# Performance work log

Hardware: AMD Instinct MI355X
Metric: run time of the kernel (lower is better)

The kernel has to match this reference:

```python
import jax, jax.numpy as jnp
import numpy as np

B, S, V, D, E, L = 4, 256, 50000, 300, 128, 20  # batch, seq, vocab, embed, encoder_size, labels


def _gru(x, h0, wih, whh, bih, bhh):
    """Unidirectional torch-style GRU. x: [B,S,Din], h0: [B,H]. Returns ([B,S,H], [B,H])."""
    gx = jnp.einsum('bsd,hd->bsh', x, wih) + bih  # precompute all input projections [B,S,3H]

    def step(h, gx_t):
        gh = h @ whh.T + bhh
        xr, xz, xn = jnp.split(gx_t, 3, axis=-1)
        hr, hz, hn = jnp.split(gh, 3, axis=-1)
        r = jax.nn.sigmoid(xr + hr)
        z = jax.nn.sigmoid(xz + hz)
        n = jnp.tanh(xn + r * hn)
        h2 = (1.0 - z) * n + z * h
        return h2, h2

    hT, hs = jax.lax.scan(step, h0, jnp.swapaxes(gx, 0, 1))
    return jnp.swapaxes(hs, 0, 1), hT


def _bigru(x, h0, pf, pb):
    """Bidirectional GRU. h0: [2,B,H]. Returns ([B,S,2H], [2,B,H])."""
    of, hf = _gru(x, h0[0], *pf)
    ob, hb = _gru(x[:, ::-1], h0[1], *pb)
    return jnp.concatenate([of, ob[:, ::-1]], axis=-1), jnp.stack([hf, hb])


def reference(inputs, emb,
              enc_wih_f, enc_whh_f, enc_bih_f, enc_bhh_f,
              enc_wih_b, enc_whh_b, enc_bih_b, enc_bhh_b,
              hid_wih_f, hid_whh_f, hid_bih_f, hid_bhh_f,
              hid_wih_b, hid_whh_b, hid_bih_b, hid_bhh_b,
              agg_wih_f, agg_whh_f, agg_bih_f, agg_bhh_f,
              agg_wih_b, agg_whh_b, agg_bih_b, agg_bhh_b,
              Wc1, Wc2, vc, Wb, Wd, vd, Wm, vm, Ws, vs, Wp, vp, Wpred):
    x = emb[inputs]                                # [B,S,D]
    b = x.shape[0]
    h0 = jnp.zeros((2, b, E), x.dtype)
    hp, hidden = _bigru(x, h0,
                        (enc_wih_f, enc_whh_f, enc_bih_f, enc_bhh_f),
                        (enc_wih_b, enc_whh_b, enc_bih_b, enc_bhh_b))   # [B,S,2E]
    hq, _ = _bigru(hp, hidden,
                   (hid_wih_f, hid_whh_f, hid_bih_f, hid_bhh_f),
                   (hid_wih_b, hid_whh_b, hid_bih_b, hid_bhh_b))        # [B,S,2E]

    # ptc: additive attention, score = vc . tanh(Wc1 hp_k + Wc2 hq_q)
    s1 = jnp.einsum('bkd,ed->bke', hp, Wc1)
    s2 = jnp.einsum('bqd,ed->bqe', hq, Wc2)
    sc = jnp.einsum('bqke,e->bqk', jnp.tanh(s1[:, None] + s2[:, :, None]), vc)
    ptc = jnp.einsum('bqk,bkd->bqd', jax.nn.softmax(sc, -1), hp)

    # ptb: bilinear attention, score = hq_q . (Wb hp_k)
    sc = jnp.einsum('bqd,bkd->bqk', hq, jnp.einsum('bkd,ed->bke', hp, Wb))
    ptb = jnp.einsum('bqk,bkd->bqd', jax.nn.softmax(sc, -1), hp)

    # ptd: score = vd . tanh(Wd (hp_k * hq_q))
    sc = jnp.einsum('bqke,e->bqk', jnp.tanh(jnp.einsum('bqkd,ed->bqke', hp[:, None] * hq[:, :, None], Wd)), vd)
    ptd = jnp.einsum('bqk,bkd->bqd', jax.nn.softmax(sc, -1), hp)

    # ptm: score = vm . tanh(Wm (hp_k - hq_q))
    sc = jnp.einsum('bqke,e->bqk', jnp.tanh(jnp.einsum('bqkd,ed->bqke', hp[:, None] - hq[:, :, None], Wm)), vm)
    ptm = jnp.einsum('bqk,bkd->bqd', jax.nn.softmax(sc, -1), hp)

    # pts: self, score = vs . tanh(Ws (hq_k * hq_q))
    sc = jnp.einsum('bqke,e->bqk', jnp.tanh(jnp.einsum('bqkd,ed->bqke', hq[:, None] * hq[:, :, None], Ws)), vs)
    pts = jnp.einsum('bqk,bkd->bqd', jax.nn.softmax(sc, -1), hq)

    agg = jnp.concatenate([hq, pts, ptc, ptd, ptb, ptm], axis=-1)  # [B,S,12E]
    agg_rep, _ = _bigru(agg, jnp.zeros((2, b, E), x.dtype),
                        (agg_wih_f, agg_whh_f, agg_bih_f, agg_bhh_f),
                        (agg_wih_b, agg_whh_b, agg_bih_b, agg_bhh_b))  # [B,S,2E]

    # pooled query rl over hq
    sj = jnp.einsum('bse,e->bs', jnp.tanh(jnp.einsum('bsd,ed->bse', hq, Wp)), vp)
    rl = jnp.einsum('bs,bsd->bd', jax.nn.softmax(sj, -1), hq)       # [B,2E]

    # final pooling over agg_rep (note: no tanh here, matching source)
    sc = jnp.einsum('bse,e->bs',
                    jnp.einsum('bsd,ed->bse', agg_rep, Wc1) + jnp.einsum('bd,ed->be', rl, Wc2)[:, None],
                    vc)
    rr = jnp.einsum('bs,bsd->bd', jax.nn.softmax(sc, -1), agg_rep)  # [B,2E]
    return jax.nn.sigmoid(rr @ Wpred.T)                              # [B,labels]


def setup_inputs() -> dict:
    key = jax.random.key(0)
    ks = iter(jax.random.split(key, 64))
    f = lambda *s: jax.random.normal(next(ks), s, jnp.float32) * 0.05
    H3 = 3 * E
    return dict(
        inputs=jax.random.randint(next(ks), (B, S), 0, V),
        emb=f(V, D),
        enc_wih_f=f(H3, D), enc_whh_f=f(H3, E), enc_bih_f=f(H3), enc_bhh_f=f(H3),
        enc_wih_b=f(H3, D), enc_whh_b=f(H3, E), enc_bih_b=f(H3), enc_bhh_b=f(H3),
        hid_wih_f=f(H3, 2 * E), hid_whh_f=f(H3, E), hid_bih_f=f(H3), hid_bhh_f=f(H3),
        hid_wih_b=f(H3, 2 * E), hid_whh_b=f(H3, E), hid_bih_b=f(H3), hid_bhh_b=f(H3),
        agg_wih_f=f(H3, 12 * E), agg_whh_f=f(H3, E), agg_bih_f=f(H3), agg_bhh_f=f(H3),
        agg_wih_b=f(H3, 12 * E), agg_whh_b=f(H3, E), agg_bih_b=f(H3), agg_bhh_b=f(H3),
        Wc1=f(E, 2 * E), Wc2=f(E, 2 * E), vc=f(E),
        Wb=f(2 * E, 2 * E),
        Wd=f(E, 2 * E), vd=f(E),
        Wm=f(E, 2 * E), vm=f(E),
        Ws=f(E, 2 * E), vs=f(E),
        Wp=f(E, 2 * E), vp=f(E),
        Wpred=f(L, 2 * E),
    )
```

## Files before the change

### kernel.cpp

```cpp
#include <hip/hip_runtime.h>
#include <math.h>

#define BB 4
#define SS 256
#define DD 300
#define DP 304
#define EE 128
#define LL 20
#define H3 384
#define D2 256
#define D12 1536

typedef __attribute__((ext_vector_type(8)))  short short8;
typedef __attribute__((ext_vector_type(16))) float f32x16;

__device__ __forceinline__ float tanh_fast(float x){
  float e = __expf(2.f*x);
  return 1.f - 2.f/(e+1.f);
}
__device__ __forceinline__ float sigmoidf_(float x){ return 1.f/(1.f+__expf(-x)); }
__device__ __forceinline__ float bf16_to_f(unsigned u){ return __builtin_bit_cast(float, u<<16); }
__device__ __forceinline__ float bf16hi_to_f(unsigned u){ return __builtin_bit_cast(float, u & 0xFFFF0000u); }
__device__ __forceinline__ unsigned bf16_rne(float f){
  unsigned u = __builtin_bit_cast(unsigned, f);
  return (u + 0x7FFFu + ((u>>16)&1u)) >> 16;
}
__device__ __forceinline__ unsigned pack_bf16x2(float lo, float hi){
  return bf16_rne(lo) | (bf16_rne(hi)<<16);
}

__global__ void k_cvt_bf16(const float* __restrict__ src, unsigned short* __restrict__ dst, int n2){
  int i = blockIdx.x*blockDim.x + threadIdx.x;
  if (i < n2){
    float2 f = *(const float2*)(src + 2*i);
    *(unsigned*)(dst + 2*i) = pack_bf16x2(f.x, f.y);
  }
}

struct CvtSeg { const float* src; unsigned short* dst; int rows, Ks, Kd; };
struct CvtArgs { CvtSeg s[13]; };
__global__ void k_cvt_weights(CvtArgs a){
  CvtSeg sg = a.s[blockIdx.y];
  int p = blockIdx.x*256 + threadIdx.x;
  int Kd2 = sg.Kd>>1;
  int npairs = sg.rows*Kd2;
  if (p >= npairs) return;
  int row = p/Kd2, kk = (p - row*Kd2)*2;
  float f0 = (kk   < sg.Ks)? sg.src[(size_t)row*sg.Ks+kk  ] : 0.f;
  float f1 = (kk+1 < sg.Ks)? sg.src[(size_t)row*sg.Ks+kk+1] : 0.f;
  *(unsigned*)(sg.dst + (size_t)row*sg.Kd + kk) = pack_bf16x2(f0,f1);
}

__global__ void k_embed(const int* __restrict__ inp, const float* __restrict__ emb,
                        unsigned short* __restrict__ xb){
  int row = blockIdx.x;
  int idx = inp[row];
  const float* src = emb + (size_t)idx*DD;
  unsigned short* dst = xb + (size_t)row*DP;
  int p = threadIdx.x;
  if (p < DP/2){
    float f0 = (2*p   < DD)? src[2*p  ] : 0.f;
    float f1 = (2*p+1 < DD)? src[2*p+1] : 0.f;
    *(unsigned*)(dst + 2*p) = pack_bf16x2(f0,f1);
  }
}

__global__ void k_init2(float* __restrict__ gf, const float* __restrict__ bf,
                        float* __restrict__ gb, const float* __restrict__ bb){
  int row = blockIdx.x, n = threadIdx.x;
  gf[(size_t)row*H3+n] = bf[n];
  gb[(size_t)row*H3+n] = bb[n];
}

__global__ __launch_bounds__(64) void k_mmbf(
    const unsigned short* __restrict__ X, const unsigned short* __restrict__ W,
    const float* __restrict__ bias, float* __restrict__ out,
    int N, int K, int kspan){
  int lane=threadIdx.x, col=lane&31, half=lane>>5;
  int n0=blockIdx.x*32, m0=blockIdx.y*64;
  int ks=blockIdx.z*kspan, ke=ks+kspan; if (ke>K) ke=K;
  const unsigned short* pa0 = X + (size_t)(m0+col)*K + half*8;
  const unsigned short* pa1 = pa0 + (size_t)32*K;
  const unsigned short* pb  = W + (size_t)(n0+col)*K + half*8;
  f32x16 acc0={}, acc1={};
  #pragma unroll 2
  for (int k=ks;k<ke;k+=16){
    short8 a0=__builtin_bit_cast(short8, *(const uint4*)(pa0+k));
    short8 a1=__builtin_bit_cast(short8, *(const uint4*)(pa1+k));
    short8 bv=__builtin_bit_cast(short8, *(const uint4*)(pb +k));
    acc0=__builtin_amdgcn_mfma_f32_32x32x16_bf16(a0,bv,acc0,0,0,0);
    acc1=__builtin_amdgcn_mfma_f32_32x32x16_bf16(a1,bv,acc1,0,0,0);
  }
  int cn = n0+col;
  if (gridDim.z==1){
    float bn = bias? bias[cn] : 0.f;
    #pragma unroll
    for (int r=0;r<16;r++){
      int row=(r&3)+8*(r>>2)+4*half;
      out[(size_t)(m0+row)*N+cn]    = acc0[r]+bn;
      out[(size_t)(m0+32+row)*N+cn] = acc1[r]+bn;
    }
  } else {
    #pragma unroll
    for (int r=0;r<16;r++){
      int row=(r&3)+8*(r>>2)+4*half;
      atomicAdd(&out[(size_t)(m0+row)*N+cn],    acc0[r]);
      atomicAdd(&out[(size_t)(m0+32+row)*N+cn], acc1[r]);
    }
  }
}

__global__ __launch_bounds__(512, 1) void k_gru_scan(const float* __restrict__ gxf, const float* __restrict__ gxb,
                          const float* __restrict__ whhf, const float* __restrict__ whhb,
                          const float* __restrict__ bhhf, const float* __restrict__ bhhb,
                          const float* __restrict__ h0,
                          float* __restrict__ out,
                          float* __restrict__ hT){
  int b=blockIdx.x, dir=blockIdx.y, tid=threadIdx.x;
  const float* gx  = dir? gxb : gxf;
  const float* whh = dir? whhb : whhf;
  const float* bhh = dir? bhhb : bhhf;
  int r = tid>>2, part = tid&3, phase = r&7;
  float4 w_r[8], w_z[8], w_n[8];
  #pragma unroll
  for (int j=0;j<8;j++){
    int jj=(j+phase)&7;
    int off = part*32 + jj*4;
    w_r[j] = *(const float4*)&whh[(size_t)r*EE        + off];
    w_z[j] = *(const float4*)&whh[(size_t)(r+128)*EE  + off];
    w_n[j] = *(const float4*)&whh[(size_t)(r+256)*EE  + off];
  }
  float b_r=bhh[r], b_z=bhh[r+128], b_n=bhh[r+256];
  __shared__ __align__(16) float h[2][EE];
  float hprev = h0? h0[((size_t)dir*BB+b)*EE + r] : 0.f;
  if (part==0) h[0][r] = hprev;
  float xr=0.f,xz=0.f,xn=0.f;
  {
    int s0 = dir? (SS-1) : 0;
    const float* g0 = gx + ((size_t)b*SS+s0)*H3;
    if (part==0){ xr=g0[r]; xz=g0[EE+r]; xn=g0[2*EE+r]; }
  }
  __syncthreads();
  int cur=0;
  for (int t=0;t<SS;t++){
    int s = dir? (SS-1-t) : t;
    float ar=0.f, az=0.f, an=0.f;
    #pragma unroll
    for (int j=0;j<8;j++){
      int jj=(j+phase)&7;
      float4 hv = *(const float4*)&h[cur][part*32 + jj*4];
      ar += w_r[j].x*hv.x + w_r[j].y*hv.y + w_r[j].z*hv.z + w_r[j].w*hv.w;
      az += w_z[j].x*hv.x + w_z[j].y*hv.y + w_z[j].z*hv.z + w_z[j].w*hv.w;
      an += w_n[j].x*hv.x + w_n[j].y*hv.y + w_n[j].z*hv.z + w_n[j].w*hv.w;
    }
    ar += __shfl_xor(ar,1); ar += __shfl_xor(ar,2);
    az += __shfl_xor(az,1); az += __shfl_xor(az,2);
    an += __shfl_xor(an,1); an += __shfl_xor(an,2);
    if (part==0){
      float rg = sigmoidf_(xr + ar + b_r);
      float zg = sigmoidf_(xz + az + b_z);
      float ng = tanh_fast(xn + rg*(an + b_n));
      float h2 = (1.f-zg)*ng + zg*hprev;
      hprev = h2;
      h[cur^1][r] = h2;
      out[((size_t)b*SS+s)*D2 + dir*EE + r] = h2;
      if (t+1<SS){
        int sn = dir? (SS-2-t) : (t+1);
        const float* gn = gx + ((size_t)b*SS+sn)*H3;
        xr=gn[r]; xz=gn[EE+r]; xn=gn[2*EE+r];
      }
    }
    cur^=1;
    __syncthreads();
  }
  if (hT && part==0) hT[((size_t)dir*BB+b)*EE+r]=hprev;
}

__global__ void k_copy_hq(const unsigned short* __restrict__ hqb, unsigned short* __restrict__ aggb){
  int row=blockIdx.x;
  aggb[(size_t)row*D12 + threadIdx.x] = hqb[(size_t)row*D2 + threadIdx.x];
}

__device__ __forceinline__ void softmax256(float val, float* red, float* p){
  int tid=threadIdx.x;
  red[tid]=val; __syncthreads();
  for (int st=128; st>0; st>>=1){ if (tid<st) red[tid]=fmaxf(red[tid],red[tid+st]); __syncthreads(); }
  float mx=red[0]; __syncthreads();
  float ex=__expf(val-mx); red[tid]=ex; __syncthreads();
  for (int st=128; st>0; st>>=1){ if (tid<st) red[tid]+=red[tid+st]; __syncthreads(); }
  float inv=1.f/red[0];
  p[tid]=ex*inv; __syncthreads();
}

__global__ __launch_bounds__(256) void k_attn_add(const float* __restrict__ A, const float* __restrict__ Bq,
                          const float* __restrict__ v, float sign,
                          const float* __restrict__ V, unsigned short* __restrict__ aggout, int off){
  __shared__ __align__(16) float bq[EE];
  __shared__ __align__(16) float vv[EE];
  __shared__ float p[SS]; __shared__ float red[SS];
  int q=blockIdx.x, b=blockIdx.y, tid=threadIdx.x;
  if (tid<EE){ bq[tid]=sign*Bq[((size_t)b*SS+q)*EE+tid]; vv[tid]=v[tid]; }
  __syncthreads();
  const float* Ar = A + ((size_t)b*SS+tid)*EE;
  float s=0.f;
  #pragma unroll
  for (int e=0;e<EE;e+=4){
    float4 a=*(const float4*)(Ar+e);
    float4 bb=*(const float4*)(bq+e);
    float4 vw=*(const float4*)(vv+e);
    s += vw.x*tanh_fast(a.x+bb.x)+vw.y*tanh_fast(a.y+bb.y)+vw.z*tanh_fast(a.z+bb.z)+vw.w*tanh_fast(a.w+bb.w);
  }
  softmax256(s, red, p);
  const float* V0 = V + (size_t)b*SS*D2;
  float o=0.f;
  for (int k=0;k<SS;k++) o += p[k]*V0[(size_t)k*D2+tid];
  aggout[((size_t)b*SS+q)*D12 + off + tid] = (unsigned short)bf16_rne(o);
}

__global__ __launch_bounds__(256) void k_attn_bil(const float* __restrict__ Pb, const float* __restrict__ hq,
                          const float* __restrict__ V, unsigned short* __restrict__ aggout, int off){
  __shared__ __align__(16) float hqq[D2];
  __shared__ float p[SS]; __shared__ float red[SS];
  int q=blockIdx.x, b=blockIdx.y, tid=threadIdx.x;
  hqq[tid]=hq[((size_t)b*SS+q)*D2+tid];
  __syncthreads();
  const float* Pr = Pb + ((size_t)b*SS+tid)*D2;
  float s=0.f;
  #pragma unroll
  for (int d=0;d<D2;d+=4){
    float4 a=*(const float4*)(Pr+d);
    float4 hh=*(const float4*)(hqq+d);
    s += a.x*hh.x+a.y*hh.y+a.z*hh.z+a.w*hh.w;
  }
  softmax256(s, red, p);
  const float* V0 = V + (size_t)b*SS*D2;
  float o=0.f;
  for (int k=0;k<SS;k++) o += p[k]*V0[(size_t)k*D2+tid];
  aggout[((size_t)b*SS+q)*D12 + off + tid] = (unsigned short)bf16_rne(o);
}

__global__ __launch_bounds__(256, 2) void k_mulattn_fused(
    const unsigned short* __restrict__ keysb,
    const float* __restrict__ qm,
    const unsigned short* __restrict__ Wb,
    const float* __restrict__ v,
    const float* __restrict__ V,
    unsigned short* __restrict__ aggout, int off){
  __shared__ __align__(16) float qrow[D2];
  __shared__ __align__(16) float vrow[EE];
  __shared__ float scq[SS];
  __shared__ float red[SS];
  __shared__ float p[SS];
  int q=blockIdx.x, b=blockIdx.y, tid=threadIdx.x;
  int wave=tid>>6, lane=tid&63;
  size_t bS = (size_t)b*SS;
  qrow[tid]=qm[(bS+q)*D2+tid];
  if (tid<EE) vrow[tid]=v[tid];
  __syncthreads();

  f32x16 acc[2][4]={};
  int m0 = wave*64;
  int col = lane&31, half = lane>>5;
  const unsigned short* krow0 = keysb + (bS + m0 + col)*D2 + half*8;
  const unsigned short* krow1 = krow0 + 32*D2;
  const unsigned short* wrow[4];
  #pragma unroll
  for (int n=0;n<4;n++) wrow[n] = Wb + (size_t)(n*32+col)*D2 + half*8;

  for (int d0=0; d0<D2; d0+=16){
    float4 qsA = *(const float4*)&qrow[d0 + half*8];
    float4 qsB = *(const float4*)&qrow[d0 + half*8 + 4];
    short8 bfrag[4];
    #pragma unroll
    for (int n=0;n<4;n++) bfrag[n] = __builtin_bit_cast(short8, *(const uint4*)(wrow[n]+d0));
    #pragma unroll
    for (int i=0;i<2;i++){
      uint4 raw = *(const uint4*)((i? krow1:krow0) + d0);
      float f0=bf16_to_f(raw.x)*qsA.x, f1=bf16hi_to_f(raw.x)*qsA.y;
      float f2=bf16_to_f(raw.y)*qsA.z, f3=bf16hi_to_f(raw.y)*qsA.w;
      float f4=bf16_to_f(raw.z)*qsB.x, f5=bf16hi_to_f(raw.z)*qsB.y;
      float f6=bf16_to_f(raw.w)*qsB.z, f7=bf16hi_to_f(raw.w)*qsB.w;
      uint4 pk;
      pk.x=pack_bf16x2(f0,f1);
      pk.y=pack_bf16x2(f2,f3);
      pk.z=pack_bf16x2(f4,f5);
      pk.w=pack_bf16x2(f6,f7);
      short8 afrag = __builtin_bit_cast(short8, pk);
      #pragma unroll
      for (int n=0;n<4;n++)
        acc[i][n] = __builtin_amdgcn_mfma_f32_32x32x16_bf16(afrag, bfrag[n], acc[i][n], 0,0,0);
    }
  }
  float vn[4];
  #pragma unroll
  for (int n=0;n<4;n++) vn[n]=vrow[n*32+col];
  #pragma unroll
  for (int i=0;i<2;i++){
    #pragma unroll
    for (int r=0;r<16;r++){
      float s = vn[0]*tanh_fast(acc[i][0][r]) + vn[1]*tanh_fast(acc[i][1][r])
              + vn[2]*tanh_fast(acc[i][2][r]) + vn[3]*tanh_fast(acc[i][3][r]);
      s += __shfl_xor(s,1,32); s += __shfl_xor(s,2,32); s += __shfl_xor(s,4,32);
      s += __shfl_xor(s,8,32); s += __shfl_xor(s,16,32);
      int k = m0 + i*32 + (r&3) + 8*(r>>2) + 4*half;
      scq[k] = s;
    }
  }
  __syncthreads();
  float val = scq[tid];
  softmax256(val, red, p);
  const float* V0 = V + bS*D2;
  float o=0.f;
  for (int k=0;k<SS;k++) o += p[k]*V0[(size_t)k*D2+tid];
  aggout[(bS+q)*D12 + off + tid] = (unsigned short)bf16_rne(o);
}

__global__ __launch_bounds__(256) void k_rl(const float* __restrict__ spj, const float* __restrict__ hq,
                    const float* __restrict__ vp, const float* __restrict__ Wc2,
                    float* __restrict__ sB){
  __shared__ __align__(16) float vpl[EE];
  __shared__ float p[SS]; __shared__ float red[SS];
  __shared__ __align__(16) float rr[D2];
  int b=blockIdx.x, tid=threadIdx.x;
  if (tid<EE) vpl[tid]=vp[tid];
  __syncthreads();
  const float* row = spj + ((size_t)b*SS+tid)*EE;
  float sj=0.f;
  #pragma unroll
  for (int e=0;e<EE;e+=4){
    float4 a=*(const float4*)(row+e);
    float4 vw=*(const float4*)(vpl+e);
    sj += vw.x*tanh_fast(a.x)+vw.y*tanh_fast(a.y)+vw.z*tanh_fast(a.z)+vw.w*tanh_fast(a.w);
  }
  softmax256(sj, red, p);
  float o=0.f;
  for (int s=0;s<SS;s++) o += p[s]*hq[((size_t)b*SS+s)*D2+tid];
  rr[tid]=o; __syncthreads();
  if (tid<EE){
    const float* wr = Wc2 + (size_t)tid*D2;
    float a=0.f;
    #pragma unroll
    for (int d=0;d<D2;d+=4){
      float4 w4=*(const float4*)(wr+d);
      float4 r4=*(const float4*)(rr+d);
      a += w4.x*r4.x+w4.y*r4.y+w4.z*r4.z+w4.w*r4.w;
    }
    sB[(size_t)b*EE+tid]=a;
  }
}

__global__ __launch_bounds__(256) void k_final(const float* __restrict__ sA, const float* __restrict__ sB,
                       const float* __restrict__ vc, const float* __restrict__ agg_rep,
                       const float* __restrict__ Wpred, float* __restrict__ out){
  __shared__ __align__(16) float sBl[EE];
  __shared__ __align__(16) float vcl[EE];
  __shared__ float p[SS]; __shared__ float red[SS]; __shared__ float rr[D2];
  int b=blockIdx.x, tid=threadIdx.x;
  if (tid<EE){ sBl[tid]=sB[(size_t)b*EE+tid]; vcl[tid]=vc[tid]; }
  __syncthreads();
  const float* rowA = sA + ((size_t)b*SS+tid)*EE;
  float sc=0.f;
  #pragma unroll
  for (int e=0;e<EE;e+=4){
    float4 a=*(const float4*)(rowA+e);
    float4 bb=*(const float4*)(sBl+e);
    float4 vw=*(const float4*)(vcl+e);
    sc += vw.x*(a.x+bb.x)+vw.y*(a.y+bb.y)+vw.z*(a.z+bb.z)+vw.w*(a.w+bb.w);
  }
  softmax256(sc, red, p);
  float o=0.f;
  for (int s=0;s<SS;s++) o += p[s]*agg_rep[((size_t)b*SS+s)*D2+tid];
  rr[tid]=o; __syncthreads();
  if (tid<LL){
    float a=0.f;
    const float* wr = Wpred + (size_t)tid*D2;
    for (int d=0;d<D2;d++) a += wr[d]*rr[d];
    out[(size_t)b*LL+tid]=sigmoidf_(a);
  }
}

extern "C" void kernel_launch(void* const* d_in, const int* in_sizes, int n_in,
                              void* d_out, int out_size, void* d_ws, size_t ws_size,
                              hipStream_t stream){
  (void)in_sizes; (void)n_in; (void)out_size; (void)ws_size;
  const int*   inp = (const int*)d_in[0];
  const float* emb = (const float*)d_in[1];
  const float* enc_wih_f=(const float*)d_in[2],  *enc_whh_f=(const float*)d_in[3],
             *enc_bih_f=(const float*)d_in[4],  *enc_bhh_f=(const float*)d_in[5];
  const float* enc_wih_b=(const float*)d_in[6],  *enc_whh_b=(const float*)d_in[7],
             *enc_bih_b=(const float*)d_in[8],  *enc_bhh_b=(const float*)d_in[9];
  const float* hid_wih_f=(const float*)d_in[10], *hid_whh_f=(const float*)d_in[11],
             *hid_bih_f=(const float*)d_in[12], *hid_bhh_f=(const float*)d_in[13];
  const float* hid_wih_b=(const float*)d_in[14], *hid_whh_b=(const float*)d_in[15],
             *hid_bih_b=(const float*)d_in[16], *hid_bhh_b=(const float*)d_in[17];
  const float* agg_wih_f=(const float*)d_in[18], *agg_whh_f=(const float*)d_in[19],
             *agg_bih_f=(const float*)d_in[20], *agg_bhh_f=(const float*)d_in[21];
  const float* agg_wih_b=(const float*)d_in[22], *agg_whh_b=(const float*)d_in[23],
             *agg_bih_b=(const float*)d_in[24], *agg_bhh_b=(const float*)d_in[25];
  const float* Wc1=(const float*)d_in[26], *Wc2=(const float*)d_in[27], *vc=(const float*)d_in[28];
  const float* Wb =(const float*)d_in[29];
  const float* Wd =(const float*)d_in[30], *vd=(const float*)d_in[31];
  const float* Wm =(const float*)d_in[32], *vm=(const float*)d_in[33];
  const float* Ws =(const float*)d_in[34], *vs=(const float*)d_in[35];
  const float* Wp =(const float*)d_in[36], *vp=(const float*)d_in[37];
  const float* Wpred=(const float*)d_in[38];

  float* ws = (float*)d_ws;
  size_t o = 0;
  float* gxf     = ws + o; o += (size_t)BB*SS*H3;
  float* gxb     = ws + o; o += (size_t)BB*SS*H3;
  float* hp      = ws + o; o += (size_t)BB*SS*D2;
  float* hq      = ws + o; o += (size_t)BB*SS*D2;
  float* hidden  = ws + o; o += (size_t)2*BB*EE;
  float* s1      = ws + o; o += (size_t)BB*SS*EE;
  float* s2      = ws + o; o += (size_t)BB*SS*EE;
  float* Am      = ws + o; o += (size_t)BB*SS*EE;
  float* Bm      = ws + o; o += (size_t)BB*SS*EE;
  float* Pb      = ws + o; o += (size_t)BB*SS*D2;
  float* spj     = ws + o; o += (size_t)BB*SS*EE;
  float* agg_rep = ws + o; o += (size_t)BB*SS*D2;
  float* sA      = ws + o; o += (size_t)BB*SS*EE;
  float* sB      = ws + o; o += (size_t)BB*EE;
  unsigned short* x_bf      = (unsigned short*)(ws+o); o += (size_t)BB*SS*DP/2;
  unsigned short* hp_bf     = (unsigned short*)(ws+o); o += (size_t)BB*SS*D2/2;
  unsigned short* hq_bf     = (unsigned short*)(ws+o); o += (size_t)BB*SS*D2/2;
  unsigned short* agg_bf    = (unsigned short*)(ws+o); o += (size_t)BB*SS*D12/2;
  unsigned short* aggrep_bf = (unsigned short*)(ws+o); o += (size_t)BB*SS*D2/2;
  unsigned short* encf_bf   = (unsigned short*)(ws+o); o += (size_t)H3*DP/2;
  unsigned short* encb_bf   = (unsigned short*)(ws+o); o += (size_t)H3*DP/2;
  unsigned short* hidf_bf   = (unsigned short*)(ws+o); o += (size_t)H3*D2/2;
  unsigned short* hidb_bf   = (unsigned short*)(ws+o); o += (size_t)H3*D2/2;
  unsigned short* aggf_bf   = (unsigned short*)(ws+o); o += (size_t)H3*D12/2;
  unsigned short* aggb_bf   = (unsigned short*)(ws+o); o += (size_t)H3*D12/2;
  unsigned short* Wc1_bf    = (unsigned short*)(ws+o); o += (size_t)EE*D2/2;
  unsigned short* Wc2_bf    = (unsigned short*)(ws+o); o += (size_t)EE*D2/2;
  unsigned short* Wm_bf     = (unsigned short*)(ws+o); o += (size_t)EE*D2/2;
  unsigned short* Wb_bf     = (unsigned short*)(ws+o); o += (size_t)D2*D2/2;
  unsigned short* Wp_bf     = (unsigned short*)(ws+o); o += (size_t)EE*D2/2;
  unsigned short* Wd_bf     = (unsigned short*)(ws+o); o += (size_t)EE*D2/2;
  unsigned short* Ws_bf     = (unsigned short*)(ws+o); o += (size_t)EE*D2/2;

  const int M = BB*SS;
  auto mmbf=[&](const unsigned short* X,const unsigned short* W,const float* bias,
                float* outp,int N,int K,int z,int kspan){
    dim3 g(N/32, M/64, z);
    k_mmbf<<<g,64,0,stream>>>(X,W,bias,outp,N,K,kspan);
  };

  k_embed<<<M,256,0,stream>>>(inp, emb, x_bf);
  CvtArgs ca;
  ca.s[0]  = {enc_wih_f, encf_bf, H3, DD, DP};
  ca.s[1]  = {enc_wih_b, encb_bf, H3, DD, DP};
  ca.s[2]  = {hid_wih_f, hidf_bf, H3, D2, D2};
  ca.s[3]  = {hid_wih_b, hidb_bf, H3, D2, D2};
  ca.s[4]  = {agg_wih_f, aggf_bf, H3, D12, D12};
  ca.s[5]  = {agg_wih_b, aggb_bf, H3, D12, D12};
  ca.s[6]  = {Wc1, Wc1_bf, EE, D2, D2};
  ca.s[7]  = {Wc2, Wc2_bf, EE, D2, D2};
  ca.s[8]  = {Wm,  Wm_bf,  EE, D2, D2};
  ca.s[9]  = {Wb,  Wb_bf,  D2, D2, D2};
  ca.s[10] = {Wp,  Wp_bf,  EE, D2, D2};
  ca.s[11] = {Wd,  Wd_bf,  EE, D2, D2};
  ca.s[12] = {Ws,  Ws_bf,  EE, D2, D2};
  {
    int maxpairs = H3*D12/2;
    dim3 g((maxpairs+255)/256, 13);
    k_cvt_weights<<<g,256,0,stream>>>(ca);
  }

  k_init2<<<M,H3,0,stream>>>(gxf, enc_bih_f, gxb, enc_bih_b);
  mmbf(x_bf, encf_bf, nullptr, gxf, H3, DP, 4, 80);
  mmbf(x_bf, encb_bf, nullptr, gxb, H3, DP, 4, 80);
  k_gru_scan<<<dim3(BB,2),512,0,stream>>>(gxf,gxb,enc_whh_f,enc_whh_b,enc_bhh_f,enc_bhh_b,
                                          nullptr,hp,hidden);
  k_cvt_bf16<<<(M*D2/2+255)/256,256,0,stream>>>(hp, hp_bf, M*D2/2);

  k_init2<<<M,H3,0,stream>>>(gxf, hid_bih_f, gxb, hid_bih_b);
  mmbf(hp_bf, hidf_bf, nullptr, gxf, H3, D2, 4, 64);
  mmbf(hp_bf, hidb_bf, nullptr, gxb, H3, D2, 4, 64);
  k_gru_scan<<<dim3(BB,2),512,0,stream>>>(gxf,gxb,hid_whh_f,hid_whh_b,hid_bhh_f,hid_bhh_b,
                                          hidden,hq,nullptr);
  k_cvt_bf16<<<(M*D2/2+255)/256,256,0,stream>>>(hq, hq_bf, M*D2/2);

  mmbf(hp_bf, Wc1_bf, nullptr, s1,  EE, D2, 1, D2);
  mmbf(hq_bf, Wc2_bf, nullptr, s2,  EE, D2, 1, D2);
  mmbf(hp_bf, Wm_bf,  nullptr, Am,  EE, D2, 1, D2);
  mmbf(hq_bf, Wm_bf,  nullptr, Bm,  EE, D2, 1, D2);
  mmbf(hp_bf, Wb_bf,  nullptr, Pb,  D2, D2, 1, D2);
  mmbf(hq_bf, Wp_bf,  nullptr, spj, EE, D2, 1, D2);

  k_copy_hq<<<M,256,0,stream>>>(hq_bf, agg_bf);
  dim3 gq(SS,BB);
  k_attn_add<<<gq,256,0,stream>>>(s1,s2,vc, 1.f, hp, agg_bf, 512);
  k_attn_add<<<gq,256,0,stream>>>(Am,Bm,vm,-1.f, hp, agg_bf, 1280);
  k_attn_bil<<<gq,256,0,stream>>>(Pb,hq,hp,agg_bf,1024);
  k_mulattn_fused<<<gq,256,0,stream>>>(hp_bf,hq,Wd_bf,vd,hp,agg_bf,768);
  k_mulattn_fused<<<gq,256,0,stream>>>(hq_bf,hq,Ws_bf,vs,hq,agg_bf,256);

  k_init2<<<M,H3,0,stream>>>(gxf, agg_bih_f, gxb, agg_bih_b);
  mmbf(agg_bf, aggf_bf, nullptr, gxf, H3, D12, 8, 192);
  mmbf(agg_bf, aggb_bf, nullptr, gxb, H3, D12, 8, 192);
  k_gru_scan<<<dim3(BB,2),512,0,stream>>>(gxf,gxb,agg_whh_f,agg_whh_b,agg_bhh_f,agg_bhh_b,
                                          nullptr,agg_rep,nullptr);
  k_cvt_bf16<<<(M*D2/2+255)/256,256,0,stream>>>(agg_rep, aggrep_bf, M*D2/2);

  k_rl<<<BB,256,0,stream>>>(spj,hq,vp,Wc2,sB);
  mmbf(aggrep_bf, Wc1_bf, nullptr, sA, EE, D2, 1, D2);
  k_final<<<BB,256,0,stream>>>(sA,sB,vc,agg_rep,Wpred,(float*)d_out);
}
```

Measured before the change: 1.182 ms.

## Keep GRU recurrent weights as bf16 in LDS and prefetch two steps ahead

The GRU scan kernel no longer holds fp32 recurrent weights in registers. The weights are converted to bf16 in the batched weight-conversion kernel and staged into padded shared memory, then read each step and unpacked with packed f32x2 math. Input-gate values are now prefetched two timesteps ahead instead of one, and the h buffer is padded to avoid bank conflicts. This frees registers and hides global load latency on the serial critical path, at the cost of bf16 rounding of the recurrent weights and extra LDS traffic every step.

```diff
diff --git a/kernel.cpp b/kernel.cpp
--- a/kernel.cpp
+++ b/kernel.cpp
@@ -10,7 +10,9 @@
 #define H3 384
 #define D2 256
 #define D12 1536
-
+#define WSTR 136
+
+typedef __attribute__((ext_vector_type(2)))  float f32x2;
 typedef __attribute__((ext_vector_type(8)))  short short8;
 typedef __attribute__((ext_vector_type(16))) float f32x16;
 
@@ -28,6 +30,10 @@
 __device__ __forceinline__ unsigned pack_bf16x2(float lo, float hi){
   return bf16_rne(lo) | (bf16_rne(hi)<<16);
 }
+__device__ __forceinline__ f32x2 upk2(unsigned u){
+  f32x2 v; v.x = __builtin_bit_cast(float, u<<16); v.y = __builtin_bit_cast(float, u & 0xFFFF0000u);
+  return v;
+}
 
 __global__ void k_cvt_bf16(const float* __restrict__ src, unsigned short* __restrict__ dst, int n2){
   int i = blockIdx.x*blockDim.x + threadIdx.x;
@@ -38,7 +44,7 @@
 }
 
 struct CvtSeg { const float* src; unsigned short* dst; int rows, Ks, Kd; };
-struct CvtArgs { CvtSeg s[13]; };
+struct CvtArgs { CvtSeg s[19]; };
 __global__ void k_cvt_weights(CvtArgs a){
   CvtSeg sg = a.s[blockIdx.y];
   int p = blockIdx.x*256 + threadIdx.x;
@@ -110,64 +116,71 @@
   }
 }
 
-__global__ __launch_bounds__(512, 1) void k_gru_scan(const float* __restrict__ gxf, const float* __restrict__ gxb,
-                          const float* __restrict__ whhf, const float* __restrict__ whhb,
+__global__ __launch_bounds__(512) void k_gru_scan(
+                          const float* __restrict__ gxf, const float* __restrict__ gxb,
+                          const unsigned short* __restrict__ whhf, const unsigned short* __restrict__ whhb,
                           const float* __restrict__ bhhf, const float* __restrict__ bhhb,
                           const float* __restrict__ h0,
                           float* __restrict__ out,
                           float* __restrict__ hT){
+  __shared__ unsigned short Wl[H3*WSTR];
+  __shared__ __align__(16) float h[2][144];
   int b=blockIdx.x, dir=blockIdx.y, tid=threadIdx.x;
   const float* gx  = dir? gxb : gxf;
-  const float* whh = dir? whhb : whhf;
+  const unsigned short* whh = dir? whhb : whhf;
   const float* bhh = dir? bhhb : bhhf;
-  int r = tid>>2, part = tid&3, phase = r&7;
-  float4 w_r[8], w_z[8], w_n[8];
-  #pragma unroll
-  for (int j=0;j<8;j++){
-    int jj=(j+phase)&7;
-    int off = part*32 + jj*4;
-    w_r[j] = *(const float4*)&whh[(size_t)r*EE        + off];
-    w_z[j] = *(const float4*)&whh[(size_t)(r+128)*EE  + off];
-    w_n[j] = *(const float4*)&whh[(size_t)(r+256)*EE  + off];
-  }
+  for (int i=tid; i<H3*16; i+=512){
+    int row=i>>4, c=i&15;
+    *(uint4*)&Wl[row*WSTR + c*8] = *(const uint4*)&whh[row*EE + c*8];
+  }
+  int r = tid>>2, part = tid&3;
+  int kb = part*32;
+  int hb = part*36;
   float b_r=bhh[r], b_z=bhh[r+128], b_n=bhh[r+256];
-  __shared__ __align__(16) float h[2][EE];
   float hprev = h0? h0[((size_t)dir*BB+b)*EE + r] : 0.f;
-  if (part==0) h[0][r] = hprev;
-  float xr=0.f,xz=0.f,xn=0.f;
-  {
-    int s0 = dir? (SS-1) : 0;
-    const float* g0 = gx + ((size_t)b*SS+s0)*H3;
-    if (part==0){ xr=g0[r]; xz=g0[EE+r]; xn=g0[2*EE+r]; }
+  if (part==0) h[0][r + ((r>>5)<<2)] = hprev;
+  float x0r=0.f,x0z=0.f,x0n=0.f, x1r=0.f,x1z=0.f,x1n=0.f;
+  if (part==0){
+    const float* g0 = gx + ((size_t)b*SS + (dir? SS-1 : 0))*H3;
+    x0r=g0[r]; x0z=g0[EE+r]; x0n=g0[2*EE+r];
+    const float* g1 = gx + ((size_t)b*SS + (dir? SS-2 : 1))*H3;
+    x1r=g1[r]; x1z=g1[EE+r]; x1n=g1[2*EE+r];
   }
   __syncthreads();
   int cur=0;
+  int wr_base = r*WSTR + kb, wz_base = (r+128)*WSTR + kb, wn_base = (r+256)*WSTR + kb;
   for (int t=0;t<SS;t++){
     int s = dir? (SS-1-t) : t;
-    float ar=0.f, az=0.f, an=0.f;
-    #pragma unroll
-    for (int j=0;j<8;j++){
-      int jj=(j+phase)&7;
-      float4 hv = *(const float4*)&h[cur][part*32 + jj*4];
-      ar += w_r[j].x*hv.x + w_r[j].y*hv.y + w_r[j].z*hv.z + w_r[j].w*hv.w;
-      az += w_z[j].x*hv.x + w_z[j].y*hv.y + w_z[j].z*hv.z + w_z[j].w*hv.w;
-      an += w_n[j].x*hv.x + w_n[j].y*hv.y + w_n[j].z*hv.z + w_n[j].w*hv.w;
-    }
-    ar += __shfl_xor(ar,1); ar += __shfl_xor(ar,2);
-    az += __shfl_xor(az,1); az += __shfl_xor(az,2);
-    an += __shfl_xor(an,1); an += __shfl_xor(an,2);
+    f32x2 ar={0.f,0.f}, az={0.f,0.f}, an={0.f,0.f};
+    #pragma unroll
+    for (int c=0;c<4;c++){
+      float4 h0v = *(const float4*)&h[cur][hb + c*8];
+      float4 h1v = *(const float4*)&h[cur][hb + c*8 + 4];
+      uint4 wwr = *(const uint4*)&Wl[wr_base + c*8];
+      uint4 wwz = *(const uint4*)&Wl[wz_base + c*8];
+      uint4 wwn = *(const uint4*)&Wl[wn_base + c*8];
+      f32x2 hA={h0v.x,h0v.y}, hB={h0v.z,h0v.w}, hC={h1v.x,h1v.y}, hD={h1v.z,h1v.w};
+      ar += upk2(wwr.x)*hA + upk2(wwr.y)*hB + upk2(wwr.z)*hC + upk2(wwr.w)*hD;
+      az += upk2(wwz.x)*hA + upk2(wwz.y)*hB + upk2(wwz.z)*hC + upk2(wwz.w)*hD;
+      an += upk2(wwn.x)*hA + upk2(wwn.y)*hB + upk2(wwn.z)*hC + upk2(wwn.w)*hD;
+    }
+    float arf = ar.x+ar.y, azf = az.x+az.y, anf = an.x+an.y;
+    arf += __shfl_xor(arf,1); arf += __shfl_xor(arf,2);
+    azf += __shfl_xor(azf,1); azf += __shfl_xor(azf,2);
+    anf += __shfl_xor(anf,1); anf += __shfl_xor(anf,2);
     if (part==0){
-      float rg = sigmoidf_(xr + ar + b_r);
-      float zg = sigmoidf_(xz + az + b_z);
-      float ng = tanh_fast(xn + rg*(an + b_n));
+      float rg = sigmoidf_(x0r + arf + b_r);
+      float zg = sigmoidf_(x0z + azf + b_z);
+      float ng = tanh_fast(x0n + rg*(anf + b_n));
       float h2 = (1.f-zg)*ng + zg*hprev;
       hprev = h2;
-      h[cur^1][r] = h2;
+      h[cur^1][r + ((r>>5)<<2)] = h2;
       out[((size_t)b*SS+s)*D2 + dir*EE + r] = h2;
-      if (t+1<SS){
-        int sn = dir? (SS-2-t) : (t+1);
+      x0r=x1r; x0z=x1z; x0n=x1n;
+      if (t+2<SS){
+        int sn = dir? (SS-3-t) : (t+2);
         const float* gn = gx + ((size_t)b*SS+sn)*H3;
-        xr=gn[r]; xz=gn[EE+r]; xn=gn[2*EE+r];
+        x1r=gn[r]; x1z=gn[EE+r]; x1n=gn[2*EE+r];
       }
     }
     cur^=1;
@@ -439,6 +452,12 @@
   unsigned short* Wp_bf     = (unsigned short*)(ws+o); o += (size_t)EE*D2/2;
   unsigned short* Wd_bf     = (unsigned short*)(ws+o); o += (size_t)EE*D2/2;
   unsigned short* Ws_bf     = (unsigned short*)(ws+o); o += (size_t)EE*D2/2;
+  unsigned short* ewhf_bf   = (unsigned short*)(ws+o); o += (size_t)H3*EE/2;
+  unsigned short* ewhb_bf   = (unsigned short*)(ws+o); o += (size_t)H3*EE/2;
+  unsigned short* hwhf_bf   = (unsigned short*)(ws+o); o += (size_t)H3*EE/2;
+  unsigned short* hwhb_bf   = (unsigned short*)(ws+o); o += (size_t)H3*EE/2;
+  unsigned short* awhf_bf   = (unsigned short*)(ws+o); o += (size_t)H3*EE/2;
+  unsigned short* awhb_bf   = (unsigned short*)(ws+o); o += (size_t)H3*EE/2;
 
   const int M = BB*SS;
   auto mmbf=[&](const unsigned short* X,const unsigned short* W,const float* bias,
@@ -462,23 +481,29 @@
   ca.s[10] = {Wp,  Wp_bf,  EE, D2, D2};
   ca.s[11] = {Wd,  Wd_bf,  EE, D2, D2};
   ca.s[12] = {Ws,  Ws_bf,  EE, D2, D2};
+  ca.s[13] = {enc_whh_f, ewhf_bf, H3, EE, EE};
+  ca.s[14] = {enc_whh_b, ewhb_bf, H3, EE, EE};
+  ca.s[15] = {hid_whh_f, hwhf_bf, H3, EE, EE};
+  ca.s[16] = {hid_whh_b, hwhb_bf, H3, EE, EE};
+  ca.s[17] = {agg_whh_f, awhf_bf, H3, EE, EE};
+  ca.s[18] = {agg_whh_b, awhb_bf, H3, EE, EE};
   {
     int maxpairs = H3*D12/2;
-    dim3 g((maxpairs+255)/256, 13);
+    dim3 g((maxpairs+255)/256, 19);
     k_cvt_weights<<<g,256,0,stream>>>(ca);
   }
 
   k_init2<<<M,H3,0,stream>>>(gxf, enc_bih_f, gxb, enc_bih_b);
   mmbf(x_bf, encf_bf, nullptr, gxf, H3, DP, 4, 80);
   mmbf(x_bf, encb_bf, nullptr, gxb, H3, DP, 4, 80);
-  k_gru_scan<<<dim3(BB,2),512,0,stream>>>(gxf,gxb,enc_whh_f,enc_whh_b,enc_bhh_f,enc_bhh_b,
+  k_gru_scan<<<dim3(BB,2),512,0,stream>>>(gxf,gxb,ewhf_bf,ewhb_bf,enc_bhh_f,enc_bhh_b,
                                           nullptr,hp,hidden);
   k_cvt_bf16<<<(M*D2/2+255)/256,256,0,stream>>>(hp, hp_bf, M*D2/2);
 
   k_init2<<<M,H3,0,stream>>>(gxf, hid_bih_f, gxb, hid_bih_b);
   mmbf(hp_bf, hidf_bf, nullptr, gxf, H3, D2, 4, 64);
   mmbf(hp_bf, hidb_bf, nullptr, gxb, H3, D2, 4, 64);
-  k_gru_scan<<<dim3(BB,2),512,0,stream>>>(gxf,gxb,hid_whh_f,hid_whh_b,hid_bhh_f,hid_bhh_b,
+  k_gru_scan<<<dim3(BB,2),512,0,stream>>>(gxf,gxb,hwhf_bf,hwhb_bf,hid_bhh_f,hid_bhh_b,
                                           hidden,hq,nullptr);
   k_cvt_bf16<<<(M*D2/2+255)/256,256,0,stream>>>(hq, hq_bf, M*D2/2);
 
@@ -500,7 +525,7 @@
   k_init2<<<M,H3,0,stream>>>(gxf, agg_bih_f, gxb, agg_bih_b);
   mmbf(agg_bf, aggf_bf, nullptr, gxf, H3, D12, 8, 192);
   mmbf(agg_bf, aggb_bf, nullptr, gxb, H3, D12, 8, 192);
-  k_gru_scan<<<dim3(BB,2),512,0,stream>>>(gxf,gxb,agg_whh_f,agg_whh_b,agg_bhh_f,agg_bhh_b,
+  k_gru_scan<<<dim3(BB,2),512,0,stream>>>(gxf,gxb,awhf_bf,awhb_bf,agg_bhh_f,agg_bhh_b,
                                           nullptr,agg_rep,nullptr);
   k_cvt_bf16<<<(M*D2/2+255)/256,256,0,stream>>>(agg_rep, aggrep_bf, M*D2/2);
 
```

Result: slower. 1.501 ms (+27.0%).
